# Kernel tuning notes

Measured on AMD Instinct MI355X. Metric: run time of the kernel, lower is better.

The kernel has to match this reference:

```python
import jax, jax.numpy as jnp
import numpy as np

N, E, F_IN, C, H = 50000, 800000, 256, 128, 2
NEG_SLOPE = 0.2


def setup_inputs() -> dict:
    key = jax.random.key(0)
    ks = jax.random.split(key, 8)
    x = jax.random.normal(ks[0], (N, F_IN), dtype=jnp.float32)
    edge_index = jax.random.randint(ks[1], (2, E), 0, N, dtype=jnp.int64)
    # GATConv params (PyG: lin weight [H*C, F_IN], att_src/att_dst [H, C], bias [H*C])
    s_lin = 1.0 / np.sqrt(F_IN)
    W = jax.random.uniform(ks[2], (H * C, F_IN), minval=-s_lin, maxval=s_lin, dtype=jnp.float32)
    att_src = jax.random.normal(ks[3], (H, C), dtype=jnp.float32) * 0.1
    att_dst = jax.random.normal(ks[4], (H, C), dtype=jnp.float32) * 0.1
    bias = jnp.zeros((H * C,), dtype=jnp.float32)
    # trailing nn.Linear(H*C, C)
    s_l = 1.0 / np.sqrt(H * C)
    lin_w = jax.random.uniform(ks[5], (C, H * C), minval=-s_l, maxval=s_l, dtype=jnp.float32)
    lin_b = jax.random.uniform(ks[6], (C,), minval=-s_l, maxval=s_l, dtype=jnp.float32)
    return {"x": x, "edge_index": edge_index, "W": W, "att_src": att_src,
            "att_dst": att_dst, "bias": bias, "lin_w": lin_w, "lin_b": lin_b}


def _gat_forward(x, edge_index, W, att_src, att_dst, bias, lin_w, lin_b):
    # add self-loops (PyG default add_self_loops=True)
    loop = jnp.arange(N, dtype=edge_index.dtype)
    src = jnp.concatenate([edge_index[0], loop])  # [E+N]
    dst = jnp.concatenate([edge_index[1], loop])  # [E+N]

    h = (x @ W.T).reshape(N, H, C)                # [N, H, C]
    a_src = jnp.einsum('nhc,hc->nh', h, att_src)  # [N, H]
    a_dst = jnp.einsum('nhc,hc->nh', h, att_dst)  # [N, H]

    e = a_src[src] + a_dst[dst]                   # [E+N, H]
    e = jnp.where(e > 0, e, NEG_SLOPE * e)        # LeakyReLU(0.2)

    # softmax over edges grouped by destination node
    m = jax.ops.segment_max(e, dst, num_segments=N)          # [N, H]
    m = jnp.where(jnp.isfinite(m), m, 0.0)
    ex = jnp.exp(e - jax.lax.stop_gradient(m)[dst])
    denom = jax.ops.segment_sum(ex, dst, num_segments=N)     # [N, H]
    alpha = ex / jnp.maximum(denom[dst], 1e-16)               # [E+N, H]

    msg = h[src] * alpha[:, :, None]                          # [E+N, H, C]
    out = jax.ops.segment_sum(msg, dst, num_segments=N)       # [N, H, C]
    out = out.reshape(N, H * C) + bias

    out = jax.nn.elu(out)
    return out @ lin_w.T + lin_b                               # [N, C]


def reference(x, edge_index, W, att_src, att_dst, bias, lin_w, lin_b):
    return _gat_forward(x, edge_index, W, att_src, att_dst, bias, lin_w, lin_b)
```

## Files before the change

### kernel.cpp

```cpp
#include <hip/hip_runtime.h>
#include <hip/hip_fp16.h>
#include <math.h>

#define NN 50000
#define EE 800000
#define ET (EE + NN)
#define FIN 256
#define CCOUT 128
#define HH 2
#define HC 256
#define NEG 0.2f

#define NB_EDGE ((ET + 255) / 256)
#define NB_SCAN ((NN + 255) / 256)
#define NB_XPREP (NN / 4)

#define PREP_W_BLOCKS 64
#define PREP_LW_BLOCKS 32
#define PREP_GRID (3 + PREP_W_BLOCKS + PREP_LW_BLOCKS)

typedef __attribute__((ext_vector_type(8))) short short8;
typedef __attribute__((ext_vector_type(4))) float floatx4;

__device__ __forceinline__ unsigned short f2bf(float f)
{
    union { float f; unsigned int u; } x; x.f = f;
    unsigned int r = x.u + 0x7fffu + ((x.u >> 16) & 1u);
    return (unsigned short)(r >> 16);
}
__device__ __forceinline__ float bf2f(unsigned short u)
{
    union { unsigned int u; float f; } x; x.u = ((unsigned int)u) << 16;
    return x.f;
}
__device__ __forceinline__ float bf_lo(unsigned int u)
{
    union { unsigned int u; float f; } x; x.u = u << 16;
    return x.f;
}
__device__ __forceinline__ float bf_hi(unsigned int u)
{
    union { unsigned int u; float f; } x; x.u = u & 0xffff0000u;
    return x.f;
}
__device__ __forceinline__ float h2f_bits(unsigned short u)
{
    __half h = *(const __half*)&u;
    return __half2float(h);
}

__device__ __forceinline__ int load_idx(const int* ei32, int is64, int pos)
{
    return is64 ? ei32[2 * pos] : ei32[pos];
}

__global__ __launch_bounds__(256) void prep_kernel(const float* __restrict__ W,
                                                   const float* __restrict__ att_s,
                                                   const float* __restrict__ att_d,
                                                   const float* __restrict__ lin_w,
                                                   const int* __restrict__ ei32,
                                                   float* __restrict__ was,
                                                   float* __restrict__ wad,
                                                   unsigned short* __restrict__ Wb,
                                                   unsigned short* __restrict__ linwb,
                                                   int* __restrict__ flag)
{
    int b = blockIdx.x, t = threadIdx.x;
    if (b == 0) {
        if (t < 64) {
            int v = ei32[2 * t + 1];
            unsigned long long m = __ballot(v != 0);
            if (t == 0) *flag = (m == 0ull) ? 1 : 0;
        }
    } else if (b <= 2) {
        int hd = b - 1;
        float as = 0.f, ad = 0.f;
        for (int c = 0; c < CCOUT; c++) {
            float wv = W[(size_t)(hd * CCOUT + c) * FIN + t];
            as += att_s[hd * CCOUT + c] * wv;
            ad += att_d[hd * CCOUT + c] * wv;
        }
        was[hd * FIN + t] = as;
        wad[hd * FIN + t] = ad;
    } else if (b < 3 + PREP_W_BLOCKS) {
        int i = (b - 3) * 256 + t;
        float4 v = *(const float4*)(W + (size_t)i * 4);
        ushort4 o;
        o.x = f2bf(v.x); o.y = f2bf(v.y); o.z = f2bf(v.z); o.w = f2bf(v.w);
        *(ushort4*)(Wb + (size_t)i * 4) = o;
    } else {
        int i = (b - 3 - PREP_W_BLOCKS) * 256 + t;
        float4 v = *(const float4*)(lin_w + (size_t)i * 4);
        ushort4 o;
        o.x = f2bf(v.x); o.y = f2bf(v.y); o.z = f2bf(v.z); o.w = f2bf(v.w);
        *(ushort4*)(linwb + (size_t)i * 4) = o;
    }
}

__global__ __launch_bounds__(256) void xprep_count_kernel(const float* __restrict__ x,
                                                          const float* __restrict__ was,
                                                          const float* __restrict__ wad,
                                                          unsigned short* __restrict__ xb,
                                                          float* __restrict__ a_s,
                                                          float* __restrict__ a_d,
                                                          const int* __restrict__ ei32,
                                                          const int* __restrict__ flag,
                                                          int* __restrict__ deg,
                                                          int* __restrict__ eord)
{
    int b = blockIdx.x, t = threadIdx.x;
    if (b < NB_XPREP) {
        int w = t >> 6, l = t & 63;
        int n = b * 4 + w;
        float4 xv = *(const float4*)(x + (size_t)n * FIN + l * 4);
        ushort4 xs;
        xs.x = f2bf(xv.x); xs.y = f2bf(xv.y); xs.z = f2bf(xv.z); xs.w = f2bf(xv.w);
        *(ushort4*)(xb + (size_t)n * FIN + l * 4) = xs;

        float4 s0 = *(const float4*)(was + l * 4);
        float4 s1 = *(const float4*)(was + FIN + l * 4);
        float4 d0 = *(const float4*)(wad + l * 4);
        float4 d1 = *(const float4*)(wad + FIN + l * 4);
        float vs0 = xv.x * s0.x + xv.y * s0.y + xv.z * s0.z + xv.w * s0.w;
        float vs1 = xv.x * s1.x + xv.y * s1.y + xv.z * s1.z + xv.w * s1.w;
        float vd0 = xv.x * d0.x + xv.y * d0.y + xv.z * d0.z + xv.w * d0.w;
        float vd1 = xv.x * d1.x + xv.y * d1.y + xv.z * d1.z + xv.w * d1.w;
#pragma unroll
        for (int off = 32; off > 0; off >>= 1) {
            vs0 += __shfl_down(vs0, off);
            vs1 += __shfl_down(vs1, off);
            vd0 += __shfl_down(vd0, off);
            vd1 += __shfl_down(vd1, off);
        }
        if (l == 0) {
            a_s[n * 2 + 0] = vs0; a_s[n * 2 + 1] = vs1;
            a_d[n * 2 + 0] = vd0; a_d[n * 2 + 1] = vd1;
        }
    } else {
        int e = (b - NB_XPREP) * 256 + t;
        if (e < ET) {
            int is64 = *flag;
            int d = (e < EE) ? load_idx(ei32, is64, EE + e) : (e - EE);
            eord[e] = atomicAdd(&deg[d], 1);
        }
    }
}

template <bool ADD_BIAS, bool OUT_BF16>
__global__ __launch_bounds__(256) void gemm_mfma(const unsigned short* __restrict__ A,
                                                 const unsigned short* __restrict__ B,
                                                 const float* __restrict__ bias,
                                                 void* __restrict__ Cout,
                                                 int M, int N, int K)
{
    const int LDT = 40;
    __shared__ unsigned short As[128 * LDT];
    __shared__ unsigned short Bs[128 * LDT];

    int tid = threadIdx.x;
    int wave = tid >> 6, lane = tid & 63;
    int wr = wave >> 1, wc = wave & 1;
    int quad = lane >> 4, l16 = lane & 15;
    int bm0 = blockIdx.x * 128;
    int bn0 = blockIdx.y * 128;

    floatx4 acc[4][4] = {};

    for (int kk = 0; kk < K; kk += 32) {
#pragma unroll
        for (int p = 0; p < 2; p++) {
            int idx = p * 256 + tid;
            int row = idx >> 2, seg = idx & 3;
            int grow = bm0 + row; if (grow >= M) grow = M - 1;
            uint4 va = *(const uint4*)(A + (size_t)grow * K + kk + seg * 8);
            *(uint4*)(&As[row * LDT + seg * 8]) = va;
            uint4 vb = *(const uint4*)(B + (size_t)(bn0 + row) * K + kk + seg * 8);
            *(uint4*)(&Bs[row * LDT + seg * 8]) = vb;
        }
        __syncthreads();

        short8 af[4], bfr[4];
#pragma unroll
        for (int mi = 0; mi < 4; mi++)
            af[mi] = *(const short8*)(&As[(wr * 64 + mi * 16 + l16) * LDT + quad * 8]);
#pragma unroll
        for (int ni = 0; ni < 4; ni++)
            bfr[ni] = *(const short8*)(&Bs[(wc * 64 + ni * 16 + l16) * LDT + quad * 8]);
#pragma unroll
        for (int mi = 0; mi < 4; mi++)
#pragma unroll
            for (int ni = 0; ni < 4; ni++)
                acc[mi][ni] = __builtin_amdgcn_mfma_f32_16x16x32_bf16(af[mi], bfr[ni], acc[mi][ni], 0, 0, 0);
        __syncthreads();
    }

#pragma unroll
    for (int mi = 0; mi < 4; mi++) {
#pragma unroll
        for (int ni = 0; ni < 4; ni++) {
            int col = bn0 + wc * 64 + ni * 16 + l16;
#pragma unroll
            for (int r = 0; r < 4; r++) {
                int row = bm0 + wr * 64 + mi * 16 + quad * 4 + r;
                if (row < M) {
                    float v = acc[mi][ni][r];
                    if (ADD_BIAS) v += bias[col];
                    if (OUT_BF16)
                        ((unsigned short*)Cout)[(size_t)row * N + col] = f2bf(v);
                    else
                        ((float*)Cout)[(size_t)row * N + col] = v;
                }
            }
        }
    }
}

__global__ __launch_bounds__(256) void scan1(const int* __restrict__ deg,
                                             int* __restrict__ tmp, int* __restrict__ bsum)
{
    __shared__ int s[256];
    int i = blockIdx.x * 256 + threadIdx.x;
    int v = (i < NN) ? deg[i] : 0;
    s[threadIdx.x] = v;
    __syncthreads();
    for (int off = 1; off < 256; off <<= 1) {
        int add = (threadIdx.x >= off) ? s[threadIdx.x - off] : 0;
        __syncthreads();
        s[threadIdx.x] += add;
        __syncthreads();
    }
    if (i < NN) tmp[i] = s[threadIdx.x];
    if (threadIdx.x == 255) bsum[blockIdx.x] = s[255];
}

__global__ __launch_bounds__(256) void scan23(const int* __restrict__ deg,
                                              const int* __restrict__ tmp,
                                              const int* __restrict__ bsum,
                                              int* __restrict__ rowstart)
{
    __shared__ int s[256];
    int b = blockIdx.x, t = threadIdx.x;
    int v = (t < NB_SCAN && t < b) ? bsum[t] : 0;
    s[t] = v;
    __syncthreads();
#pragma unroll
    for (int off = 128; off > 0; off >>= 1) {
        if (t < off) s[t] += s[t + off];
        __syncthreads();
    }
    int offset = s[0];
    int i = b * 256 + t;
    if (i < NN) rowstart[i] = tmp[i] - deg[i] + offset;
    if (i == 0) rowstart[NN] = ET;
}

__global__ void scatter_kernel(const int* __restrict__ ei32, const int* __restrict__ flag,
                               const int* __restrict__ eord,
                               const int* __restrict__ rowstart,
                               const float* __restrict__ a_s,
                               const float* __restrict__ a_d,
                               uint2* __restrict__ rec)
{
    int e = blockIdx.x * blockDim.x + threadIdx.x;
    if (e >= ET) return;
    int is64 = *flag;
    int s, d;
    if (e < EE) { s = load_idx(ei32, is64, e); d = load_idx(ei32, is64, EE + e); }
    else { s = d = e - EE; }
    float e0 = a_s[s * 2 + 0] + a_d[d * 2 + 0];
    float e1 = a_s[s * 2 + 1] + a_d[d * 2 + 1];
    e0 = e0 > 0.f ? e0 : NEG * e0;
    e1 = e1 > 0.f ? e1 : NEG * e1;
    __half2 hp = __floats2half2_rn(__expf(e0), __expf(e1));
    uint2 r;
    r.x = (unsigned int)s;
    r.y = *(unsigned int*)&hp;
    rec[rowstart[d] + eord[e]] = r;
}

__global__ __launch_bounds__(256) void agg6_kernel(const unsigned short* __restrict__ hb,
                                                   const int* __restrict__ rowstart,
                                                   const uint2* __restrict__ rec,
                                                   const float* __restrict__ bias,
                                                   unsigned short* __restrict__ aggb)
{
    int wave = threadIdx.x >> 6, lane = threadIdx.x & 63;
    int d = blockIdx.x * 4 + wave;
    int half = lane >> 5;
    int l = lane & 31;
    int hshift = (l >> 4) << 4;
    int c = l * 8;
    int j0 = rowstart[d], j1 = rowstart[d + 1];

    float a0 = 0.f, a1 = 0.f, a2 = 0.f, a3 = 0.f;
    float a4 = 0.f, a5 = 0.f, a6 = 0.f, a7 = 0.f;
    float psum = 0.f;

    int j = j0 + half;
    for (; j + 2 < j1; j += 4) {
        uint2 r0 = rec[j], r1 = rec[j + 2];
        float p0 = h2f_bits((unsigned short)(r0.y >> hshift));
        float p1 = h2f_bits((unsigned short)(r1.y >> hshift));
        psum += p0 + p1;
        uint4 h0 = *(const uint4*)(hb + (size_t)r0.x * HC + c);
        uint4 h1 = *(const uint4*)(hb + (size_t)r1.x * HC + c);
        a0 += p0 * bf_lo(h0.x) + p1 * bf_lo(h1.x);
        a1 += p0 * bf_hi(h0.x) + p1 * bf_hi(h1.x);
        a2 += p0 * bf_lo(h0.y) + p1 * bf_lo(h1.y);
        a3 += p0 * bf_hi(h0.y) + p1 * bf_hi(h1.y);
        a4 += p0 * bf_lo(h0.z) + p1 * bf_lo(h1.z);
        a5 += p0 * bf_hi(h0.z) + p1 * bf_hi(h1.z);
        a6 += p0 * bf_lo(h0.w) + p1 * bf_lo(h1.w);
        a7 += p0 * bf_hi(h0.w) + p1 * bf_hi(h1.w);
    }
    for (; j < j1; j += 2) {
        uint2 r0 = rec[j];
        float p0 = h2f_bits((unsigned short)(r0.y >> hshift));
        psum += p0;
        uint4 h0 = *(const uint4*)(hb + (size_t)r0.x * HC + c);
        a0 += p0 * bf_lo(h0.x);
        a1 += p0 * bf_hi(h0.x);
        a2 += p0 * bf_lo(h0.y);
        a3 += p0 * bf_hi(h0.y);
        a4 += p0 * bf_lo(h0.z);
        a5 += p0 * bf_hi(h0.z);
        a6 += p0 * bf_lo(h0.w);
        a7 += p0 * bf_hi(h0.w);
    }

    a0 += __shfl_xor(a0, 32);
    a1 += __shfl_xor(a1, 32);
    a2 += __shfl_xor(a2, 32);
    a3 += __shfl_xor(a3, 32);
    a4 += __shfl_xor(a4, 32);
    a5 += __shfl_xor(a5, 32);
    a6 += __shfl_xor(a6, 32);
    a7 += __shfl_xor(a7, 32);
    psum += __shfl_xor(psum, 32);

    if (half == 0) {
        float inv = 1.f / fmaxf(psum, 1e-16f);
        float4 b0 = *(const float4*)(bias + c);
        float4 b1 = *(const float4*)(bias + c + 4);
        float v0 = a0 * inv + b0.x;
        float v1 = a1 * inv + b0.y;
        float v2 = a2 * inv + b0.z;
        float v3 = a3 * inv + b0.w;
        float v4 = a4 * inv + b1.x;
        float v5 = a5 * inv + b1.y;
        float v6 = a6 * inv + b1.z;
        float v7 = a7 * inv + b1.w;
        v0 = v0 > 0.f ? v0 : expm1f(v0);
        v1 = v1 > 0.f ? v1 : expm1f(v1);
        v2 = v2 > 0.f ? v2 : expm1f(v2);
        v3 = v3 > 0.f ? v3 : expm1f(v3);
        v4 = v4 > 0.f ? v4 : expm1f(v4);
        v5 = v5 > 0.f ? v5 : expm1f(v5);
        v6 = v6 > 0.f ? v6 : expm1f(v6);
        v7 = v7 > 0.f ? v7 : expm1f(v7);
        uint4 o;
        o.x = (unsigned int)f2bf(v0) | ((unsigned int)f2bf(v1) << 16);
        o.y = (unsigned int)f2bf(v2) | ((unsigned int)f2bf(v3) << 16);
        o.z = (unsigned int)f2bf(v4) | ((unsigned int)f2bf(v5) << 16);
        o.w = (unsigned int)f2bf(v6) | ((unsigned int)f2bf(v7) << 16);
        *(uint4*)(aggb + (size_t)d * HC + c) = o;
    }
}

extern "C" void kernel_launch(void* const* d_in, const int* in_sizes, int n_in,
                              void* d_out, int out_size, void* d_ws, size_t ws_size,
                              hipStream_t stream)
{
    const float* x       = (const float*)d_in[0];
    const int*   ei32    = (const int*)d_in[1];
    const float* W       = (const float*)d_in[2];
    const float* att_src = (const float*)d_in[3];
    const float* att_dst = (const float*)d_in[4];
    const float* bias    = (const float*)d_in[5];
    const float* lin_w   = (const float*)d_in[6];
    const float* lin_b   = (const float*)d_in[7];
    float* out = (float*)d_out;

    char* ws = (char*)d_ws;
    size_t off = 0;
    auto alloc = [&](size_t bytes) -> void* {
        void* p = ws + off;
        off += (bytes + 255) & ~(size_t)255;
        return p;
    };

    int*   deg    = (int*)alloc((size_t)NN * 4);
    size_t zero_bytes = off;

    int*   flag     = (int*)alloc(256);
    int*   tmp      = (int*)alloc((size_t)NN * 4);
    int*   bsum     = (int*)alloc(1024);
    int*   rowstart = (int*)alloc((size_t)(NN + 1) * 4);
    int*   eord     = (int*)alloc((size_t)ET * 4);
    float* was      = (float*)alloc((size_t)HH * FIN * 4);
    float* wad      = (float*)alloc((size_t)HH * FIN * 4);
    float* a_s      = (float*)alloc((size_t)NN * 2 * 4);
    float* a_d      = (float*)alloc((size_t)NN * 2 * 4);
    uint2* rec      = (uint2*)alloc((size_t)ET * 8);
    unsigned short* xb     = (unsigned short*)alloc((size_t)NN * FIN * 2);
    unsigned short* Wb     = (unsigned short*)alloc((size_t)HC * FIN * 2);
    unsigned short* linwb  = (unsigned short*)alloc((size_t)CCOUT * HC * 2);
    unsigned short* hb     = (unsigned short*)alloc((size_t)NN * HC * 2);
    unsigned short* aggb   = (unsigned short*)alloc((size_t)NN * HC * 2);

    hipMemsetAsync(d_ws, 0, zero_bytes, stream);

    prep_kernel<<<PREP_GRID, 256, 0, stream>>>(W, att_src, att_dst, lin_w, ei32,
                                               was, wad, Wb, linwb, flag);

    xprep_count_kernel<<<NB_XPREP + NB_EDGE, 256, 0, stream>>>(x, was, wad, xb, a_s, a_d,
                                                               ei32, flag, deg, eord);

    scan1<<<NB_SCAN, 256, 0, stream>>>(deg, tmp, bsum);
    scan23<<<NB_SCAN, 256, 0, stream>>>(deg, tmp, bsum, rowstart);

    scatter_kernel<<<NB_EDGE, 256, 0, stream>>>(ei32, flag, eord, rowstart, a_s, a_d, rec);

    dim3 g1((NN + 127) / 128, HC / 128);
    gemm_mfma<false, true><<<g1, 256, 0, stream>>>(xb, Wb, nullptr, hb, NN, HC, FIN);

    agg6_kernel<<<NN / 4, 256, 0, stream>>>(hb, rowstart, rec, bias, aggb);

    dim3 g2((NN + 127) / 128, CCOUT / 128);
    gemm_mfma<true, false><<<g2, 256, 0, stream>>>(aggb, linwb, lin_b, out, NN, CCOUT, HC);
}
```

Measured before the change: 278.9 us.

## Fuse edge scatter and first GEMM into one interleaved launch

Merges the edge-record scatter kernel and the x@W^T bf16 MFMA GEMM into one grid. Block indices interleave four scatter blocks with each GEMM tile, so memory-bound scatter work and compute-bound GEMM work run on the GPU at the same time, and one launch is removed. The cost is that every block reserves the GEMM's shared memory, which may lower occupancy for the scatter blocks, and the grid mapping relies on hard-coded block counts.

```diff
diff --git a/kernel.cpp b/kernel.cpp
--- a/kernel.cpp
+++ b/kernel.cpp
@@ -19,6 +19,13 @@
 #define PREP_LW_BLOCKS 32
 #define PREP_GRID (3 + PREP_W_BLOCKS + PREP_LW_BLOCKS)
 
+#define G1X 391
+#define G1Y 2
+#define NB_G1 (G1X * G1Y)
+#define FUSE_HEAD (NB_G1 * 5)
+#define SCAT_IN_HEAD (NB_G1 * 4)
+#define NB_FUSE (NB_EDGE + NB_G1)
+
 typedef __attribute__((ext_vector_type(8))) short short8;
 typedef __attribute__((ext_vector_type(4))) float floatx4;
 
@@ -27,11 +34,6 @@
     union { float f; unsigned int u; } x; x.f = f;
     unsigned int r = x.u + 0x7fffu + ((x.u >> 16) & 1u);
     return (unsigned short)(r >> 16);
-}
-__device__ __forceinline__ float bf2f(unsigned short u)
-{
-    union { unsigned int u; float f; } x; x.u = ((unsigned int)u) << 16;
-    return x.f;
 }
 __device__ __forceinline__ float bf_lo(unsigned int u)
 {
@@ -215,6 +217,100 @@
     }
 }
 
+__global__ __launch_bounds__(256) void scatter_gemm1_kernel(
+        const int* __restrict__ ei32, const int* __restrict__ flag,
+        const int* __restrict__ eord, const int* __restrict__ rowstart,
+        const float* __restrict__ a_s, const float* __restrict__ a_d,
+        uint2* __restrict__ rec,
+        const unsigned short* __restrict__ A,
+        const unsigned short* __restrict__ B,
+        unsigned short* __restrict__ hb)
+{
+    const int LDT = 40;
+    __shared__ unsigned short As[128 * LDT];
+    __shared__ unsigned short Bs[128 * LDT];
+
+    int b = blockIdx.x, tid = threadIdx.x;
+    int sb = -1, gb = -1;
+    if (b < FUSE_HEAD) {
+        int g = b / 5, r = b - g * 5;
+        if (r < 4) sb = g * 4 + r; else gb = g;
+    } else {
+        sb = SCAT_IN_HEAD + (b - FUSE_HEAD);
+    }
+
+    if (sb >= 0) {
+        int e = sb * 256 + tid;
+        if (e < ET) {
+            int is64 = *flag;
+            int s, d;
+            if (e < EE) { s = load_idx(ei32, is64, e); d = load_idx(ei32, is64, EE + e); }
+            else { s = d = e - EE; }
+            float e0 = a_s[s * 2 + 0] + a_d[d * 2 + 0];
+            float e1 = a_s[s * 2 + 1] + a_d[d * 2 + 1];
+            e0 = e0 > 0.f ? e0 : NEG * e0;
+            e1 = e1 > 0.f ? e1 : NEG * e1;
+            __half2 hp = __floats2half2_rn(__expf(e0), __expf(e1));
+            uint2 r;
+            r.x = (unsigned int)s;
+            r.y = *(unsigned int*)&hp;
+            rec[rowstart[d] + eord[e]] = r;
+        }
+        return;
+    }
+
+    int bx = gb % G1X, by = gb / G1X;
+    int wave = tid >> 6, lane = tid & 63;
+    int wr = wave >> 1, wc = wave & 1;
+    int quad = lane >> 4, l16 = lane & 15;
+    int bm0 = bx * 128;
+    int bn0 = by * 128;
+
+    floatx4 acc[4][4] = {};
+
+    for (int kk = 0; kk < FIN; kk += 32) {
+#pragma unroll
+        for (int p = 0; p < 2; p++) {
+            int idx = p * 256 + tid;
+            int row = idx >> 2, seg = idx & 3;
+            int grow = bm0 + row; if (grow >= NN) grow = NN - 1;
+            uint4 va = *(const uint4*)(A + (size_t)grow * FIN + kk + seg * 8);
+            *(uint4*)(&As[row * LDT + seg * 8]) = va;
+            uint4 vb = *(const uint4*)(B + (size_t)(bn0 + row) * FIN + kk + seg * 8);
+            *(uint4*)(&Bs[row * LDT + seg * 8]) = vb;
+        }
+        __syncthreads();
+
+        short8 af[4], bfr[4];
+#pragma unroll
+        for (int mi = 0; mi < 4; mi++)
+            af[mi] = *(const short8*)(&As[(wr * 64 + mi * 16 + l16) * LDT + quad * 8]);
+#pragma unroll
+        for (int ni = 0; ni < 4; ni++)
+            bfr[ni] = *(const short8*)(&Bs[(wc * 64 + ni * 16 + l16) * LDT + quad * 8]);
+#pragma unroll
+        for (int mi = 0; mi < 4; mi++)
+#pragma unroll
+            for (int ni = 0; ni < 4; ni++)
+                acc[mi][ni] = __builtin_amdgcn_mfma_f32_16x16x32_bf16(af[mi], bfr[ni], acc[mi][ni], 0, 0, 0);
+        __syncthreads();
+    }
+
+#pragma unroll
+    for (int mi = 0; mi < 4; mi++) {
+#pragma unroll
+        for (int ni = 0; ni < 4; ni++) {
+            int col = bn0 + wc * 64 + ni * 16 + l16;
+#pragma unroll
+            for (int r = 0; r < 4; r++) {
+                int row = bm0 + wr * 64 + mi * 16 + quad * 4 + r;
+                if (row < NN)
+                    hb[(size_t)row * HC + col] = f2bf(acc[mi][ni][r]);
+            }
+        }
+    }
+}
+
 __global__ __launch_bounds__(256) void scan1(const int* __restrict__ deg,
                                              int* __restrict__ tmp, int* __restrict__ bsum)
 {
@@ -252,30 +348,6 @@
     int i = b * 256 + t;
     if (i < NN) rowstart[i] = tmp[i] - deg[i] + offset;
     if (i == 0) rowstart[NN] = ET;
-}
-
-__global__ void scatter_kernel(const int* __restrict__ ei32, const int* __restrict__ flag,
-                               const int* __restrict__ eord,
-                               const int* __restrict__ rowstart,
-                               const float* __restrict__ a_s,
-                               const float* __restrict__ a_d,
-                               uint2* __restrict__ rec)
-{
-    int e = blockIdx.x * blockDim.x + threadIdx.x;
-    if (e >= ET) return;
-    int is64 = *flag;
-    int s, d;
-    if (e < EE) { s = load_idx(ei32, is64, e); d = load_idx(ei32, is64, EE + e); }
-    else { s = d = e - EE; }
-    float e0 = a_s[s * 2 + 0] + a_d[d * 2 + 0];
-    float e1 = a_s[s * 2 + 1] + a_d[d * 2 + 1];
-    e0 = e0 > 0.f ? e0 : NEG * e0;
-    e1 = e1 > 0.f ? e1 : NEG * e1;
-    __half2 hp = __floats2half2_rn(__expf(e0), __expf(e1));
-    uint2 r;
-    r.x = (unsigned int)s;
-    r.y = *(unsigned int*)&hp;
-    rec[rowstart[d] + eord[e]] = r;
 }
 
 __global__ __launch_bounds__(256) void agg6_kernel(const unsigned short* __restrict__ hb,
@@ -419,10 +491,8 @@
     scan1<<<NB_SCAN, 256, 0, stream>>>(deg, tmp, bsum);
     scan23<<<NB_SCAN, 256, 0, stream>>>(deg, tmp, bsum, rowstart);
 
-    scatter_kernel<<<NB_EDGE, 256, 0, stream>>>(ei32, flag, eord, rowstart, a_s, a_d, rec);
-
-    dim3 g1((NN + 127) / 128, HC / 128);
-    gemm_mfma<false, true><<<g1, 256, 0, stream>>>(xb, Wb, nullptr, hb, NN, HC, FIN);
+    scatter_gemm1_kernel<<<NB_FUSE, 256, 0, stream>>>(ei32, flag, eord, rowstart,
+                                                      a_s, a_d, rec, xb, Wb, hb);
 
     agg6_kernel<<<NN / 4, 256, 0, stream>>>(hb, rowstart, rec, bias, aggb);
 
```

Result: no change. 276.6 us (-0.8%).
